# Performance work log

Hardware: AMD Instinct MI355X
Metric: run time of the kernel (lower is better)

## Reference

```python
import jax, jax.numpy as jnp
import numpy as np

B, L = 1024, 256
WD, AD, DD, SD, HD, NA = 128, 32, 256, 64, 256, 17
EPS = 1e-5


def setup_inputs() -> dict:
    key = jax.random.key(0)
    ks = jax.random.split(key, 14)
    rn = lambda k, shape, s=0.05: jax.random.normal(k, shape, jnp.float32) * s
    return {
        'actions': jax.random.randint(ks[0], (B, L), 0, NA),
        'obs': jax.random.normal(ks[1], (B, L, WD), jnp.float32),
        'noise': jax.random.normal(ks[2], (B, L, SD), jnp.float32),
        'emb': rn(ks[3], (NA, AD)),
        'w_in': rn(ks[4], (SD + AD, HD)), 'b_in': jnp.zeros((HD,), jnp.float32),
        'g_ln': jnp.ones((HD,), jnp.float32), 'beta_ln': jnp.zeros((HD,), jnp.float32),
        'w_ih': rn(ks[5], (HD, 3 * DD)), 'b_ih': jnp.zeros((3 * DD,), jnp.float32),
        'w_hh': rn(ks[6], (DD, 3 * DD)), 'b_hh': jnp.zeros((3 * DD,), jnp.float32),
        'w_p1': rn(ks[7], (DD, HD)), 'b_p1': jnp.zeros((HD,), jnp.float32),
        'w_p2': rn(ks[8], (HD, 2 * SD)), 'b_p2': jnp.zeros((2 * SD,), jnp.float32),
        'w_q1': rn(ks[9], (DD + WD, HD)), 'b_q1': jnp.zeros((HD,), jnp.float32),
        'w_q2': rn(ks[10], (HD, 2 * SD)), 'b_q2': jnp.zeros((2 * SD,), jnp.float32),
    }


def _ln(x, g, b):
    m = x.mean(-1, keepdims=True)
    v = ((x - m) ** 2).mean(-1, keepdims=True)
    return (x - m) / jnp.sqrt(v + EPS) * g + b


def reference(actions, obs, noise, emb, w_in, b_in, g_ln, beta_ln,
              w_ih, b_ih, w_hh, b_hh, w_p1, b_p1, w_p2, b_p2,
              w_q1, b_q1, w_q2, b_q2):
    a_emb = emb[actions]  # (B, L, AD)

    def step(carry, xs):
        h, z = carry
        a, w, eps = xs
        x = jax.nn.relu(_ln(jnp.concatenate([z, a], -1) @ w_in + b_in, g_ln, beta_ln))
        # PyTorch GRUCell gate math
        gi = x @ w_ih + b_ih
        gh = h @ w_hh + b_hh
        i_r, i_u, i_n = jnp.split(gi, 3, -1)
        h_r, h_u, h_n = jnp.split(gh, 3, -1)
        r = jax.nn.sigmoid(i_r + h_r)
        u = jax.nn.sigmoid(i_u + h_u)
        n = jnp.tanh(i_n + r * h_n)
        h_new = (1.0 - u) * n + u * h
        # prior
        pstats = jax.nn.relu(h_new @ w_p1 + b_p1) @ w_p2 + b_p2
        pm, pls = jnp.split(pstats, 2, -1)
        ps = jax.nn.softplus(pls) + 0.1
        # posterior
        qstats = jax.nn.relu(jnp.concatenate([h_new, w], -1) @ w_q1 + b_q1) @ w_q2 + b_q2
        qm, qls = jnp.split(qstats, 2, -1)
        qs = jax.nn.softplus(qls) + 0.1
        z_new = qm + qs * eps  # reparameterized sample
        out = jnp.concatenate([h_new, z_new, pm, ps, qm, qs], -1)  # (B, DD+5*SD)
        return (h_new, z_new), out

    b = actions.shape[0]
    h0 = jnp.zeros((b, DD), jnp.float32)
    z0 = jnp.zeros((b, SD), jnp.float32)
    xs = (jnp.swapaxes(a_emb, 0, 1), jnp.swapaxes(obs, 0, 1), jnp.swapaxes(noise, 0, 1))
    _, seq = jax.lax.scan(step, (h0, z0), xs)  # (L, B, 576)
    return jnp.swapaxes(seq, 0, 1)  # (B, L, DD + 5*SD) = h|z|prior_mean|prior_std|post_mean|post_std
```

## Files before the change

kernel.cpp:

```cpp
#include <hip/hip_runtime.h>
#include <hip/hip_bf16.h>


#define B_   1024
#define L_   256
#define WD_  128
#define AD_  32
#define DD_  256
#define SD_  64
#define HD_  256
#define NA_  17
#define OUT_ 576

typedef __attribute__((ext_vector_type(8))) short bf16x8;
typedef __attribute__((ext_vector_type(4))) float f32x4;
typedef __attribute__((ext_vector_type(2))) float f32x2;
typedef __attribute__((ext_vector_type(2))) unsigned u32x2;
typedef long long fp8x8;

#define OFF_WZ   0
#define OFF_WQ1W 16384
#define OFF_WQ2  49152
#define OFF_WP1  81920
#define OFF_WP2  147456
#define PK_TOTAL 180224
#define OFF_ACTP_BYTES (PK_TOTAL * 2)
#define OFF_DSCR_BYTES (OFF_ACTP_BYTES + 32768)
#define OFF_W8_BYTES   (OFF_DSCR_BYTES + 65536)
#define W8_IHR 0
#define W8_IHU 65536
#define W8_IHN 131072
#define W8_HHR 196608
#define W8_HHU 262144
#define W8_HHN 327680
#define W8_Q1H 393216

__device__ __forceinline__ short f2bf(float f) {
    union { float f; unsigned u; } v; v.f = f;
    unsigned r = (v.u + 0x7fffu + ((v.u >> 16) & 1u)) >> 16;
    return (short)r;
}
__device__ __forceinline__ unsigned cvtpk(float a, float b) {
    unsigned r;
    asm("v_cvt_pk_bf16_f32 %0, %1, %2" : "=v"(r) : "v"(a), "v"(b));
    return r;
}
__device__ __forceinline__ int pk4fp8(float a, float b, float c, float d) {
    int r = __builtin_amdgcn_cvt_pk_fp8_f32(a, b, 0, false);
    r = __builtin_amdgcn_cvt_pk_fp8_f32(c, d, r, true);
    return r;
}

__device__ __forceinline__ f32x4 mfma16(bf16x8 a, bf16x8 b, f32x4 c) {
    return __builtin_amdgcn_mfma_f32_16x16x32_bf16(a, b, c, 0, 0, 0);
}
__device__ __forceinline__ f32x4 mfma8(fp8x8 a, fp8x8 b, f32x4 c) {
    return __builtin_amdgcn_mfma_f32_16x16x32_fp8_fp8(a, b, c, 0, 0, 0);
}

__device__ __forceinline__ float sigmoidf_(float x) { return 1.f / (1.f + __expf(-x)); }
__device__ __forceinline__ float tanhf_(float x)    { return 2.f / (1.f + __expf(-2.f * x)) - 1.f; }
__device__ __forceinline__ float softplusf_(float x){ return (x > 20.f) ? x : __logf(1.f + __expf(x)); }

template<int IMM>
__device__ __forceinline__ bf16x8 gload(const short* sbase, unsigned voff) {
    bf16x8 d;
    if constexpr (IMM == 0) {
        asm volatile("global_load_dwordx4 %0, %1, %2" : "=v"(d) : "v"(voff), "s"(sbase));
    } else {
        asm volatile("global_load_dwordx4 %0, %1, %2 offset:%3"
                     : "=v"(d) : "v"(voff), "s"(sbase), "i"(IMM));
    }
    return d;
}
template<int IMM>
__device__ __forceinline__ fp8x8 gload8(const char* sbase, unsigned voff) {
    fp8x8 d;
    if constexpr (IMM == 0) {
        asm volatile("global_load_dwordx2 %0, %1, %2" : "=v"(d) : "v"(voff), "s"(sbase));
    } else {
        asm volatile("global_load_dwordx2 %0, %1, %2 offset:%3"
                     : "=v"(d) : "v"(voff), "s"(sbase), "i"(IMM));
    }
    return d;
}
__device__ __forceinline__ f32x2 gload2f(const float* sbase, unsigned voff) {
    f32x2 d;
    asm volatile("global_load_dwordx2 %0, %1, %2 nt" : "=v"(d) : "v"(voff), "s"(sbase));
    return d;
}
__device__ __forceinline__ float gload1f(const float* sbase, unsigned voff) {
    float d;
    asm volatile("global_load_dword %0, %1, %2 nt" : "=v"(d) : "v"(voff), "s"(sbase));
    return d;
}
__device__ __forceinline__ void gstore4f(float* sbase, unsigned voff, f32x4 v) {
    asm volatile("global_store_dwordx4 %0, %1, %2 nt" :: "v"(voff), "v"(v), "s"(sbase));
}
__device__ __forceinline__ void gstore1f(float* sbase, unsigned voff, float v) {
    asm volatile("global_store_dword %0, %1, %2 nt" :: "v"(voff), "v"(v), "s"(sbase));
}

#define VMW(N) do { asm volatile("s_waitcnt vmcnt(" #N ")" ::: "memory"); \
                    __builtin_amdgcn_sched_barrier(0); } while (0)
#define BAR() do { asm volatile("s_waitcnt lgkmcnt(0)" ::: "memory"); \
                   __builtin_amdgcn_s_barrier(); \
                   __builtin_amdgcn_sched_barrier(0); } while (0)

__global__ void pack_w_kernel(const float* __restrict__ W, short* __restrict__ dst,
                              int KT, int rowOff, int srcN, int total) {
    int tid = blockIdx.x * 256 + threadIdx.x;
    if (tid >= total) return;
    int j    = tid & 7;
    int lane = (tid >> 3) & 63;
    int kt   = (tid >> 9) % KT;
    int nt   = (tid >> 9) / KT;
    int k = kt * 32 + (lane >> 4) * 8 + j;
    int n = nt * 16 + (lane & 15);
    dst[tid] = f2bf(W[(size_t)(rowOff + k) * srcN + n]);
}

__global__ void pack_f8_kernel(const float* __restrict__ W, char* __restrict__ dst,
                               int KT, int rowOff, int colOff, int srcN, int total) {
    int tid = blockIdx.x * 256 + threadIdx.x;
    if (tid >= total) return;
    int j    = tid & 7;
    int lane = (tid >> 3) & 63;
    int kt   = (tid >> 9) % KT;
    int nt   = (tid >> 9) / KT;
    int k = kt * 32 + (lane >> 4) * 8 + j;
    int n = colOff + nt * 16 + (lane & 15);
    float v = W[(size_t)(rowOff + k) * srcN + n];
    int p = __builtin_amdgcn_cvt_pk_fp8_f32(v, 0.f, 0, false);
    dst[tid] = (char)(p & 0xFF);
}

__global__ void act_proj_kernel(const float* __restrict__ emb, const float* __restrict__ w_in,
                                const float* __restrict__ b_in, float* __restrict__ actp) {
    int c = threadIdx.x;
    int a = blockIdx.x;
    float s = b_in[c];
    for (int i = 0; i < AD_; ++i) s += emb[a * AD_ + i] * w_in[(SD_ + i) * HD_ + c];
    actp[a * HD_ + c] = s;
}

#define RPB 16
#define NTH 1024

struct WB { fp8x8 ri, ui, ni, rh, uh, nh; };

template<int KT>
__device__ __forceinline__ void issueK(WB& b,
        const char* s8ri, const char* s8ui, const char* s8ni,
        const char* s8rh, const char* s8uh, const char* s8nh, unsigned voff8) {
    constexpr int IMM8 = KT * 512;
    b.ri = gload8<IMM8>(s8ri, voff8);
    b.ui = gload8<IMM8>(s8ui, voff8);
    b.ni = gload8<IMM8>(s8ni, voff8);
    b.rh = gload8<IMM8>(s8rh, voff8);
    b.uh = gload8<IMM8>(s8uh, voff8);
    b.nh = gload8<IMM8>(s8nh, voff8);
}

__launch_bounds__(NTH, 4)
__global__ void scan_kernel(const int* __restrict__ actions, const float* __restrict__ obs,
                            const float* __restrict__ noise,
                            const float* __restrict__ b_ih, const float* __restrict__ b_hh,
                            const float* __restrict__ g_ln, const float* __restrict__ beta_ln,
                            const float* __restrict__ b_q1, const float* __restrict__ b_q2,
                            const short* __restrict__ wpk, const char* __restrict__ w8,
                            const float* __restrict__ actp,
                            float* __restrict__ dscr, float* __restrict__ out) {
    __shared__ __align__(16) float ps_s [16][20];
    __shared__ __align__(16) float ps_ss[16][20];
    __shared__ __align__(16) float q2p[2][16][132];
    __shared__ __align__(16) char  xF8 [4096];
    __shared__ __align__(16) char  h8a [4096];
    __shared__ __align__(16) char  h8b [4096];
    __shared__ __align__(16) short q1F [4096];
    __shared__ __align__(16) short zF  [1024];
    __shared__ __align__(16) short obsF[2048];
    __shared__ __align__(16) float bsr_l[256], bsu_l[256], bin_l[256], bhn_l[256];
    __shared__ __align__(16) float bq1_l[256], lng_l[256], lnb_l[256], bq2_l[128];
    __shared__ __align__(16) unsigned char act8_l[L_][16];
    __shared__ __align__(16) float actp_l[NA_][260];

    const int tid  = threadIdx.x;
    const int w    = tid >> 6;
    const int lane = tid & 63;
    const int lrow = lane & 15;
    const int lgrp = lane >> 4;
    const int row0 = blockIdx.x * RPB;
    const int c0   = w * 16 + lgrp * 4;
    const int foff = lane * 8;
    const int b8off = lane * 8;
    const int fwb  = (c0 >> 5) * 512 + (lrow + 16 * ((c0 >> 3) & 3)) * 8 + (c0 & 7);
    const f32x4 zero4 = {0.f, 0.f, 0.f, 0.f};

    const int wu = __builtin_amdgcn_readfirstlane(w);
    const unsigned voff16 = (unsigned)lane * 16u;
    const unsigned voff8  = (unsigned)lane * 8u;
    const short* sbwz = wpk + OFF_WZ + (wu * 2) * 512;
    const char* s8ri  = w8 + W8_IHR + (wu * 8) * 512;
    const char* s8ui  = w8 + W8_IHU + (wu * 8) * 512;
    const char* s8ni  = w8 + W8_IHN + (wu * 8) * 512;
    const char* s8rh  = w8 + W8_HHR + (wu * 8) * 512;
    const char* s8uh  = w8 + W8_HHU + (wu * 8) * 512;
    const char* s8nh  = w8 + W8_HHN + (wu * 8) * 512;
    const char* s8q1h = w8 + W8_Q1H + (wu * 8) * 512;
    const short* sbq1w = wpk + OFF_WQ1W + (wu * 4) * 512;
    const int khalf = wu >> 3;
    const short* sbq2 = wpk + OFF_WQ2 + ((wu & 7) * 8 + khalf * 4) * 512;

    const bf16x8 Wq1w0 = *(const bf16x8*)&sbq1w[0 * 512 + foff];
    const bf16x8 Wq1w1 = *(const bf16x8*)&sbq1w[1 * 512 + foff];
    const bf16x8 Wq1w2 = *(const bf16x8*)&sbq1w[2 * 512 + foff];
    const bf16x8 Wq1w3 = *(const bf16x8*)&sbq1w[3 * 512 + foff];
    asm volatile("" :: "v"(Wq1w0), "v"(Wq1w1), "v"(Wq1w2), "v"(Wq1w3));

    if (tid < 256) {
        bsr_l[tid] = b_ih[tid] + b_hh[tid];
        bsu_l[tid] = b_ih[256 + tid] + b_hh[256 + tid];
        bin_l[tid] = b_ih[512 + tid];
        bhn_l[tid] = b_hh[512 + tid];
        bq1_l[tid] = b_q1[tid];
        lng_l[tid] = g_ln[tid];
        lnb_l[tid] = beta_ln[tid];
    } else if (tid < 384) {
        bq2_l[tid - 256] = b_q2[tid - 256];
    }
    for (int i = tid; i < RPB * L_; i += NTH) {
        int r = i >> 8, tt = i & 255;
        act8_l[tt][r] = (unsigned char)actions[(row0 + r) * L_ + tt];
    }
    for (int i = tid; i < NA_ * HD_; i += NTH)
        actp_l[i >> 8][i & 255] = actp[i];
    for (int i = tid; i < 4096; i += NTH) h8a[i] = 0;
    for (int i = tid; i < 1024; i += NTH) zF[i] = 0;
    f32x4 hreg = zero4;

    unsigned obs_off = (unsigned)((row0 + w) * L_) * (WD_ * 4u) + (unsigned)lane * 8u;
    unsigned nz_off  = (unsigned)((row0 + w) * L_) * (SD_ * 4u) + (unsigned)lane * 4u;
    unsigned ho_off  = (unsigned)((row0 + lrow) * L_) * (OUT_ * 4u) + (unsigned)c0 * 4u;
    unsigned zo_off  = (unsigned)((row0 + w) * L_) * (OUT_ * 4u);
    __syncthreads();

    WB w0, w1, w2;
    fp8x8 db0, db1, db2, db3, db4, db5, db6, db7;
    bf16x8 eb0, eb1, eb2, eb3;
    bf16x8 wzb0, wzb1;
    f32x2 obsv, obsv_n;
    float nzv, nzv_n;

    obsv = gload2f(obs, obs_off);
    nzv  = gload1f(noise, nz_off);
    wzb0 = gload<0>   (sbwz, voff16);
    wzb1 = gload<1024>(sbwz, voff16);
    issueK<0>(w0, s8ri, s8ui, s8ni, s8rh, s8uh, s8nh, voff8);
    issueK<1>(w1, s8ri, s8ui, s8ni, s8rh, s8uh, s8nh, voff8);
    issueK<2>(w2, s8ri, s8ui, s8ni, s8rh, s8uh, s8nh, voff8);
    VMW(20);
    {
        unsigned doff = (unsigned)tid * 16u;
        gstore4f(dscr, doff, zero4);
        gstore4f(dscr, doff + 16384u, zero4);
        gstore4f(dscr, doff + 32768u, zero4);
        gstore4f(dscr, doff + 49152u, zero4);
    }

    for (int t = 0; t < L_; ++t) {
        const char* h8c = (t & 1) ? h8b : h8a;
        char*       h8n = (t & 1) ? h8a : h8b;

        f32x4 xp;
        {
            VMW(22);
            f32x4 a = zero4;
            a = mfma16(wzb0, *(const bf16x8*)&zF[foff], a);
            a = mfma16(wzb1, *(const bf16x8*)&zF[512 + foff], a);
            int act = act8_l[t][lrow];
            xp = a + *(const f32x4*)&actp_l[act][c0];
            float s  = xp[0] + xp[1] + xp[2] + xp[3];
            float ss = xp[0]*xp[0] + xp[1]*xp[1] + xp[2]*xp[2] + xp[3]*xp[3];
            s  += __shfl_xor(s, 16, 64);  s  += __shfl_xor(s, 32, 64);
            ss += __shfl_xor(ss, 16, 64); ss += __shfl_xor(ss, 32, 64);
            if (lgrp == 0) { ps_s[lrow][w] = s; ps_ss[lrow][w] = ss; }
            int oc = lane * 2;
            *(unsigned*)&obsF[(oc >> 5) * 512 + (w + 16 * ((oc >> 3) & 3)) * 8 + (oc & 7)]
                = cvtpk(obsv[0], obsv[1]);
        }
        BAR();

        {
            float s  = ps_s [lrow][lgrp] + ps_s [lrow][lgrp + 4]
                     + ps_s [lrow][lgrp + 8] + ps_s [lrow][lgrp + 12];
            float ss = ps_ss[lrow][lgrp] + ps_ss[lrow][lgrp + 4]
                     + ps_ss[lrow][lgrp + 8] + ps_ss[lrow][lgrp + 12];
            s  += __shfl_xor(s, 16, 64);  s  += __shfl_xor(s, 32, 64);
            ss += __shfl_xor(ss, 16, 64); ss += __shfl_xor(ss, 32, 64);
            float mean = s * (1.f / 256.f);
            float rstd = rsqrtf(ss * (1.f / 256.f) - mean * mean + 1e-5f);
            f32x4 g  = *(const f32x4*)&lng_l[c0];
            f32x4 bb = *(const f32x4*)&lnb_l[c0];
            float r0 = fmaxf((xp[0] - mean) * rstd * g[0] + bb[0], 0.f);
            float r1 = fmaxf((xp[1] - mean) * rstd * g[1] + bb[1], 0.f);
            float r2 = fmaxf((xp[2] - mean) * rstd * g[2] + bb[2], 0.f);
            float r3 = fmaxf((xp[3] - mean) * rstd * g[3] + bb[3], 0.f);
            *(int*)&xF8[fwb] = pk4fp8(r0, r1, r2, r3);
        }
        BAR();

        f32x4 ar = zero4, au = zero4, aI = zero4, aH = zero4;
#define SLOT(KT, WBUF) { \
        fp8x8 x8 = *(const fp8x8*)&xF8[(KT) * 512 + b8off]; \
        fp8x8 h8 = *(const fp8x8*)&h8c[(KT) * 512 + b8off]; \
        ar = mfma8(WBUF.ri, x8, ar); ar = mfma8(WBUF.rh, h8, ar); \
        au = mfma8(WBUF.ui, x8, au); au = mfma8(WBUF.uh, h8, au); \
        aI = mfma8(WBUF.ni, x8, aI); aH = mfma8(WBUF.nh, h8, aH); }
#define ISSUE(KT, W) issueK<KT>(W, s8ri, s8ui, s8ni, s8rh, s8uh, s8nh, voff8)

        VMW(16); SLOT(0, w0) ISSUE(3, w0);
        VMW(16); SLOT(1, w1) ISSUE(4, w1);
        VMW(16); SLOT(2, w2) ISSUE(5, w2);
        VMW(12); SLOT(3, w0) ISSUE(6, w0);
        VMW(12); SLOT(4, w1) ISSUE(7, w1);
        VMW(12); SLOT(5, w2)
        db0 = gload8<0>   (s8q1h, voff8);
        db1 = gload8<512> (s8q1h, voff8);
        db2 = gload8<1024>(s8q1h, voff8);
        db3 = gload8<1536>(s8q1h, voff8);
        VMW(10); SLOT(6, w0)
        db4 = gload8<2048>(s8q1h, voff8);
        db5 = gload8<2560>(s8q1h, voff8);
        db6 = gload8<3072>(s8q1h, voff8);
        db7 = gload8<3584>(s8q1h, voff8);
        VMW(8);  SLOT(7, w1)
        eb0 = gload<0>   (sbq2, voff16);
        eb1 = gload<1024>(sbq2, voff16);
        eb2 = gload<2048>(sbq2, voff16);
        eb3 = gload<3072>(sbq2, voff16);
        {
            unsigned onext = obs_off + ((t < L_ - 1) ? (WD_ * 4u) : 0u);
            unsigned nnext = nz_off  + ((t < L_ - 1) ? (SD_ * 4u) : 0u);
            obsv_n = gload2f(obs, onext);
            nzv_n  = gload1f(noise, nnext);
            obs_off = onext; nz_off = nnext;
        }
#undef SLOT
#undef ISSUE

        {
            f32x4 bsr = *(const f32x4*)&bsr_l[c0];
            f32x4 bsu = *(const f32x4*)&bsu_l[c0];
            f32x4 bin = *(const f32x4*)&bin_l[c0];
            f32x4 bhn = *(const f32x4*)&bhn_l[c0];
            f32x4 hv;
            #pragma unroll
            for (int j = 0; j < 4; ++j) {
                float rr = sigmoidf_(ar[j] + bsr[j]);
                float uu = sigmoidf_(au[j] + bsu[j]);
                float nn = tanhf_(aI[j] + bin[j] + rr * (aH[j] + bhn[j]));
                hv[j] = (1.f - uu) * nn + uu * hreg[j];
            }
            hreg = hv;
            *(int*)&h8n[fwb] = pk4fp8(hv[0], hv[1], hv[2], hv[3]);
        }
        BAR();

        {
            f32x4 aq = zero4;
            fp8x8 t0 = *(const fp8x8*)&h8n[0 * 512 + b8off];
            fp8x8 t1 = *(const fp8x8*)&h8n[1 * 512 + b8off];
            fp8x8 t2 = *(const fp8x8*)&h8n[2 * 512 + b8off];
            fp8x8 t3 = *(const fp8x8*)&h8n[3 * 512 + b8off];
            VMW(10);
            aq = mfma8(db0, t0, aq); aq = mfma8(db1, t1, aq);
            aq = mfma8(db2, t2, aq); aq = mfma8(db3, t3, aq);
            fp8x8 t4 = *(const fp8x8*)&h8n[4 * 512 + b8off];
            fp8x8 t5 = *(const fp8x8*)&h8n[5 * 512 + b8off];
            fp8x8 t6 = *(const fp8x8*)&h8n[6 * 512 + b8off];
            fp8x8 t7 = *(const fp8x8*)&h8n[7 * 512 + b8off];
            VMW(6);
            aq = mfma8(db4, t4, aq); aq = mfma8(db5, t5, aq);
            aq = mfma8(db6, t6, aq); aq = mfma8(db7, t7, aq);
            wzb0 = gload<0>   (sbwz, voff16);
            wzb1 = gload<1024>(sbwz, voff16);
            issueK<0>(w0, s8ri, s8ui, s8ni, s8rh, s8uh, s8nh, voff8);
            issueK<1>(w1, s8ri, s8ui, s8ni, s8rh, s8uh, s8nh, voff8);
            issueK<2>(w2, s8ri, s8ui, s8ni, s8rh, s8uh, s8nh, voff8);
            bf16x8 o0 = *(const bf16x8*)&obsF[0 * 512 + foff];
            bf16x8 o1 = *(const bf16x8*)&obsF[1 * 512 + foff];
            bf16x8 o2 = *(const bf16x8*)&obsF[2 * 512 + foff];
            bf16x8 o3 = *(const bf16x8*)&obsF[3 * 512 + foff];
            aq = mfma16(Wq1w0, o0, aq); aq = mfma16(Wq1w1, o1, aq);
            aq = mfma16(Wq1w2, o2, aq); aq = mfma16(Wq1w3, o3, aq);
            f32x4 bq = *(const f32x4*)&bq1_l[c0];
            u32x2 qb;
            qb[0] = cvtpk(fmaxf(aq[0] + bq[0], 0.f), fmaxf(aq[1] + bq[1], 0.f));
            qb[1] = cvtpk(fmaxf(aq[2] + bq[2], 0.f), fmaxf(aq[3] + bq[3], 0.f));
            *(u32x2*)&q1F[fwb] = qb;
        }
        BAR();

        {
            f32x4 a = zero4;
            VMW(22);
            bf16x8 q0 = *(const bf16x8*)&q1F[(khalf * 4 + 0) * 512 + foff];
            bf16x8 q1 = *(const bf16x8*)&q1F[(khalf * 4 + 1) * 512 + foff];
            bf16x8 q2 = *(const bf16x8*)&q1F[(khalf * 4 + 2) * 512 + foff];
            bf16x8 q3 = *(const bf16x8*)&q1F[(khalf * 4 + 3) * 512 + foff];
            a = mfma16(eb0, q0, a); a = mfma16(eb1, q1, a);
            a = mfma16(eb2, q2, a); a = mfma16(eb3, q3, a);
            *(f32x4*)&q2p[khalf][lrow][(wu & 7) * 16 + lgrp * 4] = a;
        }
        BAR();

        {
            int n = lane;
            VMW(20);
            float qm = q2p[0][w][n]      + q2p[1][w][n]      + bq2_l[n];
            float ql = q2p[0][w][64 + n] + q2p[1][w][64 + n] + bq2_l[64 + n];
            float qs = softplusf_(ql) + 0.1f;
            float zv = qm + qs * nzv;
            zF[(n >> 5) * 512 + (w + 16 * ((n >> 3) & 3)) * 8 + (n & 7)] = f2bf(zv);
            unsigned zo = zo_off;
            gstore4f(out, ho_off, hreg);
            gstore1f(out, zo + (256 + n) * 4u, zv);
            gstore1f(out, zo + (448 + n) * 4u, qm);
            gstore1f(out, zo + (512 + n) * 4u, qs);
            obsv = obsv_n;
            nzv  = nzv_n;
        }
        BAR();
        ho_off += OUT_ * 4u;
        zo_off += OUT_ * 4u;
    }
    asm volatile("s_waitcnt vmcnt(0)" ::: "memory");
}

__launch_bounds__(256, 2)
__global__ void prior_kernel(const float* __restrict__ b_p1, const float* __restrict__ b_p2,
                             const short* __restrict__ wpk, float* __restrict__ out) {
    const short* wp1 = wpk + OFF_WP1;
    const short* wp2 = wpk + OFF_WP2;
    __shared__ __align__(16) short p1b[4][16][264];
    const int tid = threadIdx.x, wid = tid >> 6, lane = tid & 63;
    const int lrow = lane & 15, lgrp = lane >> 4;
    const size_t rbase = (size_t)blockIdx.x * 64 + wid * 16;
    const f32x4 zero4 = {0.f, 0.f, 0.f, 0.f};

    f32x4 acc[16];
    #pragma unroll
    for (int nt = 0; nt < 16; ++nt) acc[nt] = zero4;
    for (int kt = 0; kt < 8; ++kt) {
        const f32x4* hp = (const f32x4*)&out[(rbase + lrow) * OUT_ + kt * 32 + lgrp * 8];
        f32x4 h0 = hp[0], h1 = hp[1];
        bf16x8 a;
        a[0] = f2bf(h0[0]); a[1] = f2bf(h0[1]); a[2] = f2bf(h0[2]); a[3] = f2bf(h0[3]);
        a[4] = f2bf(h1[0]); a[5] = f2bf(h1[1]); a[6] = f2bf(h1[2]); a[7] = f2bf(h1[3]);
        #pragma unroll
        for (int nt = 0; nt < 16; ++nt) {
            bf16x8 b = *(const bf16x8*)&wp1[(nt * 8 + kt) * 512 + lane * 8];
            acc[nt] = mfma16(a, b, acc[nt]);
        }
    }
    #pragma unroll
    for (int nt = 0; nt < 16; ++nt) {
        int colb = nt * 16 + lrow;
        #pragma unroll
        for (int j = 0; j < 4; ++j)
            p1b[wid][lgrp * 4 + j][colb] = f2bf(fmaxf(acc[nt][j] + b_p1[colb], 0.f));
    }
    __syncthreads();

    f32x4 acc2[8];
    #pragma unroll
    for (int nt = 0; nt < 8; ++nt) acc2[nt] = zero4;
    for (int kt = 0; kt < 8; ++kt) {
        bf16x8 a = *(const bf16x8*)&p1b[wid][lrow][kt * 32 + lgrp * 8];
        #pragma unroll
        for (int nt = 0; nt < 8; ++nt) {
            bf16x8 b = *(const bf16x8*)&wp2[(nt * 8 + kt) * 512 + lane * 8];
            acc2[nt] = mfma16(a, b, acc2[nt]);
        }
    }
    #pragma unroll
    for (int nt = 0; nt < 8; ++nt) {
        #pragma unroll
        for (int j = 0; j < 4; ++j) {
            size_t rw = rbase + lgrp * 4 + j;
            int col = nt * 16 + lrow;
            float v = acc2[nt][j] + b_p2[col];
            if (col < 64) out[rw * OUT_ + 320 + col] = v;
            else          out[rw * OUT_ + 384 + (col - 64)] = softplusf_(v) + 0.1f;
        }
    }
}

extern "C" void kernel_launch(void* const* d_in, const int* in_sizes, int n_in,
                              void* d_out, int out_size, void* d_ws, size_t ws_size,
                              hipStream_t stream) {
    const int*   actions = (const int*)  d_in[0];
    const float* obs     = (const float*)d_in[1];
    const float* noise   = (const float*)d_in[2];
    const float* emb     = (const float*)d_in[3];
    const float* w_in    = (const float*)d_in[4];
    const float* b_in    = (const float*)d_in[5];
    const float* g_ln    = (const float*)d_in[6];
    const float* beta_ln = (const float*)d_in[7];
    const float* w_ih    = (const float*)d_in[8];
    const float* b_ih    = (const float*)d_in[9];
    const float* w_hh    = (const float*)d_in[10];
    const float* b_hh    = (const float*)d_in[11];
    const float* w_p1    = (const float*)d_in[12];
    const float* b_p1    = (const float*)d_in[13];
    const float* w_p2    = (const float*)d_in[14];
    const float* b_p2    = (const float*)d_in[15];
    const float* w_q1    = (const float*)d_in[16];
    const float* b_q1    = (const float*)d_in[17];
    const float* w_q2    = (const float*)d_in[18];
    const float* b_q2    = (const float*)d_in[19];

    short* wpk  = (short*)d_ws;
    float* actp = (float*)((char*)d_ws + OFF_ACTP_BYTES);
    float* dscr = (float*)((char*)d_ws + OFF_DSCR_BYTES);
    char*  w8   = (char*) d_ws + OFF_W8_BYTES;
    float* out  = (float*)d_out;

    auto packLaunch = [&](const float* W, int off, int KT, int rowOff, int srcN, int total) {
        pack_w_kernel<<<(total + 255) / 256, 256, 0, stream>>>(W, wpk + off, KT, rowOff, srcN, total);
    };
    packLaunch(w_in, OFF_WZ,    2, 0,   256, 64 * 256);
    packLaunch(w_q1, OFF_WQ1W,  4, 256, 256, 128 * 256);
    packLaunch(w_q2, OFF_WQ2,   8, 0,   128, 256 * 128);
    packLaunch(w_p1, OFF_WP1,   8, 0,   256, 256 * 256);
    packLaunch(w_p2, OFF_WP2,   8, 0,   128, 256 * 128);

    auto pack8 = [&](const float* W, int dstOff, int colOff, int srcN) {
        pack_f8_kernel<<<256, 256, 0, stream>>>(W, w8 + dstOff, 8, 0, colOff, srcN, 65536);
    };
    pack8(w_ih, W8_IHR, 0,   768);
    pack8(w_ih, W8_IHU, 256, 768);
    pack8(w_ih, W8_IHN, 512, 768);
    pack8(w_hh, W8_HHR, 0,   768);
    pack8(w_hh, W8_HHU, 256, 768);
    pack8(w_hh, W8_HHN, 512, 768);
    pack8(w_q1, W8_Q1H, 0,   256);
    act_proj_kernel<<<NA_, 256, 0, stream>>>(emb, w_in, b_in, actp);

    scan_kernel<<<B_ / RPB, NTH, 0, stream>>>(actions, obs, noise, b_ih, b_hh,
                                              g_ln, beta_ln, b_q1, b_q2, wpk, w8, actp, dscr, out);
    prior_kernel<<<(B_ * L_) / 64, 256, 0, stream>>>(b_p1, b_p2, wpk, out);
}
```

Before: 2.787 ms.

## Keep GRU r/u gate weights register-resident and move Wq1 obs weights to LDS

The fp8 r and u gate weight fragments for both the input and hidden GRU matmuls are loaded once into registers, 32 fp8x8 values per lane. Only the n-gate weights are still streamed from global/L2 each step, now through a four-deep buffer. The Wq1 obs-part weights move from persistent registers into a 64KB LDS array to free VGPRs. The goal is to cut per-step weight streaming traffic and the waits on it, at the cost of higher register pressure, a larger LDS footprint, and retuned vmcnt wait counts that must match the new load ordering.

```diff
diff --git a/kernel.cpp b/kernel.cpp
--- a/kernel.cpp
+++ b/kernel.cpp
@@ -147,18 +147,13 @@
 #define RPB 16
 #define NTH 1024
 
-struct WB { fp8x8 ri, ui, ni, rh, uh, nh; };
+struct NB { fp8x8 ni, nh; };
 
 template<int KT>
-__device__ __forceinline__ void issueK(WB& b,
-        const char* s8ri, const char* s8ui, const char* s8ni,
-        const char* s8rh, const char* s8uh, const char* s8nh, unsigned voff8) {
+__device__ __forceinline__ void issueN(NB& b, const char* s8ni, const char* s8nh,
+                                       unsigned voff8) {
     constexpr int IMM8 = KT * 512;
-    b.ri = gload8<IMM8>(s8ri, voff8);
-    b.ui = gload8<IMM8>(s8ui, voff8);
     b.ni = gload8<IMM8>(s8ni, voff8);
-    b.rh = gload8<IMM8>(s8rh, voff8);
-    b.uh = gload8<IMM8>(s8uh, voff8);
     b.nh = gload8<IMM8>(s8nh, voff8);
 }
 
@@ -180,6 +175,7 @@
     __shared__ __align__(16) short q1F [4096];
     __shared__ __align__(16) short zF  [1024];
     __shared__ __align__(16) short obsF[2048];
+    __shared__ __align__(16) short wq1w_l[32768];
     __shared__ __align__(16) float bsr_l[256], bsu_l[256], bin_l[256], bhn_l[256];
     __shared__ __align__(16) float bq1_l[256], lng_l[256], lnb_l[256], bq2_l[128];
     __shared__ __align__(16) unsigned char act8_l[L_][16];
@@ -208,15 +204,29 @@
     const char* s8uh  = w8 + W8_HHU + (wu * 8) * 512;
     const char* s8nh  = w8 + W8_HHN + (wu * 8) * 512;
     const char* s8q1h = w8 + W8_Q1H + (wu * 8) * 512;
-    const short* sbq1w = wpk + OFF_WQ1W + (wu * 4) * 512;
     const int khalf = wu >> 3;
     const short* sbq2 = wpk + OFF_WQ2 + ((wu & 7) * 8 + khalf * 4) * 512;
 
-    const bf16x8 Wq1w0 = *(const bf16x8*)&sbq1w[0 * 512 + foff];
-    const bf16x8 Wq1w1 = *(const bf16x8*)&sbq1w[1 * 512 + foff];
-    const bf16x8 Wq1w2 = *(const bf16x8*)&sbq1w[2 * 512 + foff];
-    const bf16x8 Wq1w3 = *(const bf16x8*)&sbq1w[3 * 512 + foff];
-    asm volatile("" :: "v"(Wq1w0), "v"(Wq1w1), "v"(Wq1w2), "v"(Wq1w3));
+    fp8x8 Rih[8], Uih[8], Rhh[8], Uhh[8];
+#define LOADRES(arr, base) \
+    arr[0] = gload8<0>(base, voff8);    arr[1] = gload8<512>(base, voff8);  \
+    arr[2] = gload8<1024>(base, voff8); arr[3] = gload8<1536>(base, voff8); \
+    arr[4] = gload8<2048>(base, voff8); arr[5] = gload8<2560>(base, voff8); \
+    arr[6] = gload8<3072>(base, voff8); arr[7] = gload8<3584>(base, voff8);
+    LOADRES(Rih, s8ri)
+    LOADRES(Uih, s8ui)
+    LOADRES(Rhh, s8rh)
+    LOADRES(Uhh, s8uh)
+#undef LOADRES
+    asm volatile("s_waitcnt vmcnt(0)" ::: "memory");
+    asm volatile("" :: "v"(Rih[0]), "v"(Rih[1]), "v"(Rih[2]), "v"(Rih[3]),
+                       "v"(Rih[4]), "v"(Rih[5]), "v"(Rih[6]), "v"(Rih[7]));
+    asm volatile("" :: "v"(Uih[0]), "v"(Uih[1]), "v"(Uih[2]), "v"(Uih[3]),
+                       "v"(Uih[4]), "v"(Uih[5]), "v"(Uih[6]), "v"(Uih[7]));
+    asm volatile("" :: "v"(Rhh[0]), "v"(Rhh[1]), "v"(Rhh[2]), "v"(Rhh[3]),
+                       "v"(Rhh[4]), "v"(Rhh[5]), "v"(Rhh[6]), "v"(Rhh[7]));
+    asm volatile("" :: "v"(Uhh[0]), "v"(Uhh[1]), "v"(Uhh[2]), "v"(Uhh[3]),
+                       "v"(Uhh[4]), "v"(Uhh[5]), "v"(Uhh[6]), "v"(Uhh[7]));
 
     if (tid < 256) {
         bsr_l[tid] = b_ih[tid] + b_hh[tid];
@@ -235,6 +245,8 @@
     }
     for (int i = tid; i < NA_ * HD_; i += NTH)
         actp_l[i >> 8][i & 255] = actp[i];
+    for (int i = tid; i < 16384; i += NTH)
+        ((int*)wq1w_l)[i] = ((const int*)(wpk + OFF_WQ1W))[i];
     for (int i = tid; i < 4096; i += NTH) h8a[i] = 0;
     for (int i = tid; i < 1024; i += NTH) zF[i] = 0;
     f32x4 hreg = zero4;
@@ -245,7 +257,7 @@
     unsigned zo_off  = (unsigned)((row0 + w) * L_) * (OUT_ * 4u);
     __syncthreads();
 
-    WB w0, w1, w2;
+    NB n0, n1, n2, n3;
     fp8x8 db0, db1, db2, db3, db4, db5, db6, db7;
     bf16x8 eb0, eb1, eb2, eb3;
     bf16x8 wzb0, wzb1;
@@ -256,10 +268,11 @@
     nzv  = gload1f(noise, nz_off);
     wzb0 = gload<0>   (sbwz, voff16);
     wzb1 = gload<1024>(sbwz, voff16);
-    issueK<0>(w0, s8ri, s8ui, s8ni, s8rh, s8uh, s8nh, voff8);
-    issueK<1>(w1, s8ri, s8ui, s8ni, s8rh, s8uh, s8nh, voff8);
-    issueK<2>(w2, s8ri, s8ui, s8ni, s8rh, s8uh, s8nh, voff8);
-    VMW(20);
+    issueN<0>(n0, s8ni, s8nh, voff8);
+    issueN<1>(n1, s8ni, s8nh, voff8);
+    issueN<2>(n2, s8ni, s8nh, voff8);
+    issueN<3>(n3, s8ni, s8nh, voff8);
+    VMW(10);
     {
         unsigned doff = (unsigned)tid * 16u;
         gstore4f(dscr, doff, zero4);
@@ -274,7 +287,7 @@
 
         f32x4 xp;
         {
-            VMW(22);
+            VMW(12);
             f32x4 a = zero4;
             a = mfma16(wzb0, *(const bf16x8*)&zF[foff], a);
             a = mfma16(wzb1, *(const bf16x8*)&zF[512 + foff], a);
@@ -311,30 +324,29 @@
         BAR();
 
         f32x4 ar = zero4, au = zero4, aI = zero4, aH = zero4;
-#define SLOT(KT, WBUF) { \
+#define SLOT(KT, NBUF) { \
         fp8x8 x8 = *(const fp8x8*)&xF8[(KT) * 512 + b8off]; \
         fp8x8 h8 = *(const fp8x8*)&h8c[(KT) * 512 + b8off]; \
-        ar = mfma8(WBUF.ri, x8, ar); ar = mfma8(WBUF.rh, h8, ar); \
-        au = mfma8(WBUF.ui, x8, au); au = mfma8(WBUF.uh, h8, au); \
-        aI = mfma8(WBUF.ni, x8, aI); aH = mfma8(WBUF.nh, h8, aH); }
-#define ISSUE(KT, W) issueK<KT>(W, s8ri, s8ui, s8ni, s8rh, s8uh, s8nh, voff8)
-
-        VMW(16); SLOT(0, w0) ISSUE(3, w0);
-        VMW(16); SLOT(1, w1) ISSUE(4, w1);
-        VMW(16); SLOT(2, w2) ISSUE(5, w2);
-        VMW(12); SLOT(3, w0) ISSUE(6, w0);
-        VMW(12); SLOT(4, w1) ISSUE(7, w1);
-        VMW(12); SLOT(5, w2)
+        ar = mfma8(Rih[KT], x8, ar); ar = mfma8(Rhh[KT], h8, ar); \
+        au = mfma8(Uih[KT], x8, au); au = mfma8(Uhh[KT], h8, au); \
+        aI = mfma8(NBUF.ni, x8, aI); aH = mfma8(NBUF.nh, h8, aH); }
+
+        VMW(10); SLOT(0, n0) issueN<4>(n0, s8ni, s8nh, voff8);
+        VMW(10); SLOT(1, n1) issueN<5>(n1, s8ni, s8nh, voff8);
+        VMW(10); SLOT(2, n2) issueN<6>(n2, s8ni, s8nh, voff8);
+        VMW(10); SLOT(3, n3) issueN<7>(n3, s8ni, s8nh, voff8);
+        VMW(6);  SLOT(4, n0)
         db0 = gload8<0>   (s8q1h, voff8);
         db1 = gload8<512> (s8q1h, voff8);
         db2 = gload8<1024>(s8q1h, voff8);
         db3 = gload8<1536>(s8q1h, voff8);
-        VMW(10); SLOT(6, w0)
+        VMW(8);  SLOT(5, n1)
         db4 = gload8<2048>(s8q1h, voff8);
         db5 = gload8<2560>(s8q1h, voff8);
         db6 = gload8<3072>(s8q1h, voff8);
         db7 = gload8<3584>(s8q1h, voff8);
-        VMW(8);  SLOT(7, w1)
+        VMW(10); SLOT(6, n2)
+        VMW(8);  SLOT(7, n3)
         eb0 = gload<0>   (sbq2, voff16);
         eb1 = gload<1024>(sbq2, voff16);
         eb2 = gload<2048>(sbq2, voff16);
@@ -347,7 +359,6 @@
             obs_off = onext; nz_off = nnext;
         }
 #undef SLOT
-#undef ISSUE
 
         {
             f32x4 bsr = *(const f32x4*)&bsr_l[c0];
@@ -385,15 +396,16 @@
             aq = mfma8(db6, t6, aq); aq = mfma8(db7, t7, aq);
             wzb0 = gload<0>   (sbwz, voff16);
             wzb1 = gload<1024>(sbwz, voff16);
-            issueK<0>(w0, s8ri, s8ui, s8ni, s8rh, s8uh, s8nh, voff8);
-            issueK<1>(w1, s8ri, s8ui, s8ni, s8rh, s8uh, s8nh, voff8);
-            issueK<2>(w2, s8ri, s8ui, s8ni, s8rh, s8uh, s8nh, voff8);
-            bf16x8 o0 = *(const bf16x8*)&obsF[0 * 512 + foff];
-            bf16x8 o1 = *(const bf16x8*)&obsF[1 * 512 + foff];
-            bf16x8 o2 = *(const bf16x8*)&obsF[2 * 512 + foff];
-            bf16x8 o3 = *(const bf16x8*)&obsF[3 * 512 + foff];
-            aq = mfma16(Wq1w0, o0, aq); aq = mfma16(Wq1w1, o1, aq);
-            aq = mfma16(Wq1w2, o2, aq); aq = mfma16(Wq1w3, o3, aq);
+            issueN<0>(n0, s8ni, s8nh, voff8);
+            issueN<1>(n1, s8ni, s8nh, voff8);
+            issueN<2>(n2, s8ni, s8nh, voff8);
+            issueN<3>(n3, s8ni, s8nh, voff8);
+            #pragma unroll
+            for (int kk = 0; kk < 4; ++kk) {
+                bf16x8 ow = *(const bf16x8*)&wq1w_l[(wu * 4 + kk) * 512 + foff];
+                bf16x8 of = *(const bf16x8*)&obsF[kk * 512 + foff];
+                aq = mfma16(ow, of, aq);
+            }
             f32x4 bq = *(const f32x4*)&bq1_l[c0];
             u32x2 qb;
             qb[0] = cvtpk(fmaxf(aq[0] + bq[0], 0.f), fmaxf(aq[1] + bq[1], 0.f));
@@ -404,7 +416,7 @@
 
         {
             f32x4 a = zero4;
-            VMW(22);
+            VMW(12);
             bf16x8 q0 = *(const bf16x8*)&q1F[(khalf * 4 + 0) * 512 + foff];
             bf16x8 q1 = *(const bf16x8*)&q1F[(khalf * 4 + 1) * 512 + foff];
             bf16x8 q2 = *(const bf16x8*)&q1F[(khalf * 4 + 2) * 512 + foff];
@@ -417,7 +429,7 @@
 
         {
             int n = lane;
-            VMW(20);
+            VMW(10);
             float qm = q2p[0][w][n]      + q2p[1][w][n]      + bq2_l[n];
             float ql = q2p[0][w][64 + n] + q2p[1][w][64 + n] + bq2_l[64 + n];
             float qs = softplusf_(ql) + 0.1f;
```

After: 3.547 ms. 27.3% more time.
